# Kernel tuning notes

Measured on AMD Instinct MI355X. Metric: run time of the kernel, lower is better.

Reference implementation:

```python
import jax, jax.numpy as jnp
import numpy as np

B, L, D, K = 8, 256, 256, 64  # batch, slots, n_input, attn_dimension


def setup_inputs() -> dict:
    key = jax.random.key(0)
    k1, k2, k3 = jax.random.split(key, 3)
    inputs = jax.random.normal(k1, (B, L, D), dtype=jnp.float32)
    # torch.nn.Linear weights are [out_features, in_features]; scale to avoid tanh saturation
    W1 = jax.random.normal(k2, (K, 2 * D), dtype=jnp.float32) * (1.0 / np.sqrt(2 * D))
    W2 = jax.random.normal(k3, (1, K), dtype=jnp.float32) * (1.0 / np.sqrt(K))
    return {"inputs": inputs, "W1": W1, "W2": W2}


def reference(inputs, W1, W2):
    # CONCAT branch of SlotAttention:
    #   score[b,i,j] = W2 @ tanh(W1 @ concat(inputs[b,i], inputs[b,j]))
    # Split W1 into the halves acting on the i-part and j-part of the concat
    # (identical math, avoids materializing the [B,L,L,2D] concat tensor).
    d = inputs.shape[-1]
    W1i, W1j = W1[:, :d], W1[:, d:]
    qi = jnp.einsum('bld,kd->blk', inputs, W1i)          # [B,L,K]
    kj = jnp.einsum('bld,kd->blk', inputs, W1j)          # [B,L,K]
    h = jnp.tanh(qi[:, :, None, :] + kj[:, None, :, :])  # [B,L,L,K]
    scores = jnp.einsum('bijk,k->bij', h, W2[0])         # [B,L,L]
    attn = jax.nn.softmax(scores, axis=2)                # softmax over j
    context = jnp.einsum('bij,bjd->bid', attn, inputs)   # [B,L,D]
    return jnp.concatenate([inputs, context], axis=2)    # [B,L,2D]
```

## Files before the change

kernel.cpp:

```cpp
#include <hip/hip_runtime.h>


#define Bn 8
#define Ln 256
#define Dn 256
#define Kn 64
#define ROWS (Bn*Ln)
#define IPB 4

__global__ __launch_bounds__(128) void proj_kernel(
    const float* __restrict__ X,
    const float* __restrict__ W1,
    float* __restrict__ QK)
{
    __shared__ float Xs[4 * 256];
    const int tid = threadIdx.x;
    const int r0 = blockIdx.x * 4;

    const float4* Xg4 = (const float4*)(X + r0 * Dn);
    float4* Xs4 = (float4*)Xs;
    #pragma unroll
    for (int idx = tid; idx < 256; idx += 128) Xs4[idx] = Xg4[idx];
    __syncthreads();

    const int k = tid & 63, half = tid >> 6;
    const float4* Wrow = (const float4*)(W1 + k * (2 * Dn) + half * Dn);
    float acc[4] = {0, 0, 0, 0};
    #pragma unroll 8
    for (int d4 = 0; d4 < 64; ++d4) {
        float4 w = Wrow[d4];
        #pragma unroll
        for (int r = 0; r < 4; ++r) {
            float4 x = ((const float4*)(Xs + r * Dn))[d4];
            float a = acc[r];
            a = fmaf(w.x, x.x, a);
            a = fmaf(w.y, x.y, a);
            a = fmaf(w.z, x.z, a);
            a = fmaf(w.w, x.w, a);
            acc[r] = a;
        }
    }
    #pragma unroll
    for (int r = 0; r < 4; ++r)
        QK[(r0 + r) * 128 + tid] = __expf(2.0f * acc[r]);
}

__global__ __launch_bounds__(256) void attn_kernel(
    const float* __restrict__ X,
    const float* __restrict__ QK,
    const float* __restrict__ W2,
    float* __restrict__ out)
{
    __shared__ float eq_s[IPB * Kn];
    __shared__ float w2_s[Kn];
    __shared__ float S[Ln * IPB];
    __shared__ float4 red[4 * IPB * 64];

    const int tid = threadIdx.x;
    const int b  = blockIdx.x / (Ln / IPB);
    const int i0 = (blockIdx.x % (Ln / IPB)) * IPB;

    if (tid < Kn) w2_s[tid] = W2[tid];
    {
        int ii = tid >> 6, kk = tid & 63;
        eq_s[ii * Kn + kk] = QK[(b * Ln + i0 + ii) * 128 + kk];
    }

    float ekr[Kn];
    const float4* kj4 = (const float4*)(QK + (b * Ln + tid) * 128 + 64);
    #pragma unroll
    for (int q = 0; q < 16; ++q) {
        float4 v = kj4[q];
        ekr[q * 4 + 0] = v.x; ekr[q * 4 + 1] = v.y;
        ekr[q * 4 + 2] = v.z; ekr[q * 4 + 3] = v.w;
    }
    __syncthreads();

    float Wsum;
    {
        float v = w2_s[tid & 63];
        #pragma unroll
        for (int off = 32; off > 0; off >>= 1)
            v += __shfl_xor(v, off);
        Wsum = v;
    }

    float s[IPB] = {0, 0, 0, 0};
    const float4* w4  = (const float4*)w2_s;
    const float4* q4a = (const float4*)(eq_s);
    const float4* q4b = (const float4*)(eq_s + Kn);
    const float4* q4c = (const float4*)(eq_s + 2 * Kn);
    const float4* q4d = (const float4*)(eq_s + 3 * Kn);
    #pragma unroll
    for (int k4 = 0; k4 < 16; ++k4) {
        float4 w  = w4[k4];
        float4 q0 = q4a[k4], q1 = q4b[k4], q2 = q4c[k4], q3 = q4d[k4];
        #pragma unroll
        for (int c = 0; c < 4; ++c) {
            float ek = ekr[k4 * 4 + c];
            float wk = (c == 0) ? w.x : (c == 1) ? w.y : (c == 2) ? w.z : w.w;
            float e0 = (c == 0) ? q0.x : (c == 1) ? q0.y : (c == 2) ? q0.z : q0.w;
            float e1 = (c == 0) ? q1.x : (c == 1) ? q1.y : (c == 2) ? q1.z : q1.w;
            float e2 = (c == 0) ? q2.x : (c == 1) ? q2.y : (c == 2) ? q2.z : q2.w;
            float e3 = (c == 0) ? q3.x : (c == 1) ? q3.y : (c == 2) ? q3.z : q3.w;
            s[0] = fmaf(wk, __builtin_amdgcn_rcpf(fmaf(e0, ek, 1.0f)), s[0]);
            s[1] = fmaf(wk, __builtin_amdgcn_rcpf(fmaf(e1, ek, 1.0f)), s[1]);
            s[2] = fmaf(wk, __builtin_amdgcn_rcpf(fmaf(e2, ek, 1.0f)), s[2]);
            s[3] = fmaf(wk, __builtin_amdgcn_rcpf(fmaf(e3, ek, 1.0f)), s[3]);
        }
    }
    ((float4*)S)[tid] = make_float4(fmaf(-2.0f, s[0], Wsum),
                                    fmaf(-2.0f, s[1], Wsum),
                                    fmaf(-2.0f, s[2], Wsum),
                                    fmaf(-2.0f, s[3], Wsum));
    __syncthreads();

    {
        const int wv = tid >> 6, lane = tid & 63;
        float v0 = S[(lane      ) * IPB + wv];
        float v1 = S[(lane +  64) * IPB + wv];
        float v2 = S[(lane + 128) * IPB + wv];
        float v3 = S[(lane + 192) * IPB + wv];
        float m = fmaxf(fmaxf(v0, v1), fmaxf(v2, v3));
        #pragma unroll
        for (int off = 32; off > 0; off >>= 1)
            m = fmaxf(m, __shfl_xor(m, off));
        float e0 = __expf(v0 - m), e1 = __expf(v1 - m);
        float e2 = __expf(v2 - m), e3 = __expf(v3 - m);
        float sum = e0 + e1 + e2 + e3;
        #pragma unroll
        for (int off = 32; off > 0; off >>= 1)
            sum += __shfl_xor(sum, off);
        float inv = 1.0f / sum;
        S[(lane      ) * IPB + wv] = e0 * inv;
        S[(lane +  64) * IPB + wv] = e1 * inv;
        S[(lane + 128) * IPB + wv] = e2 * inv;
        S[(lane + 192) * IPB + wv] = e3 * inv;
    }
    __syncthreads();

    {
        const int wv = tid >> 6, lane = tid & 63;
        float4 acc0 = {0,0,0,0}, acc1 = {0,0,0,0}, acc2 = {0,0,0,0}, acc3 = {0,0,0,0};
        const float4* Xb4 = (const float4*)(X + b * Ln * Dn);
        const float4* S4  = (const float4*)S;
        const int jbase = wv * 64;
        #pragma unroll 8
        for (int jj = 0; jj < 64; ++jj) {
            int j = jbase + jj;
            float4 at = S4[j];
            float4 x  = Xb4[j * 64 + lane];
            acc0.x = fmaf(at.x, x.x, acc0.x); acc0.y = fmaf(at.x, x.y, acc0.y);
            acc0.z = fmaf(at.x, x.z, acc0.z); acc0.w = fmaf(at.x, x.w, acc0.w);
            acc1.x = fmaf(at.y, x.x, acc1.x); acc1.y = fmaf(at.y, x.y, acc1.y);
            acc1.z = fmaf(at.y, x.z, acc1.z); acc1.w = fmaf(at.y, x.w, acc1.w);
            acc2.x = fmaf(at.z, x.x, acc2.x); acc2.y = fmaf(at.z, x.y, acc2.y);
            acc2.z = fmaf(at.z, x.z, acc2.z); acc2.w = fmaf(at.z, x.w, acc2.w);
            acc3.x = fmaf(at.w, x.x, acc3.x); acc3.y = fmaf(at.w, x.y, acc3.y);
            acc3.z = fmaf(at.w, x.z, acc3.z); acc3.w = fmaf(at.w, x.w, acc3.w);
        }
        red[(wv * IPB + 0) * 64 + lane] = acc0;
        red[(wv * IPB + 1) * 64 + lane] = acc1;
        red[(wv * IPB + 2) * 64 + lane] = acc2;
        red[(wv * IPB + 3) * 64 + lane] = acc3;
    }
    __syncthreads();

    {
        const int i = tid >> 6, q = tid & 63;
        float4 p0 = red[(0 * IPB + i) * 64 + q];
        float4 p1 = red[(1 * IPB + i) * 64 + q];
        float4 p2 = red[(2 * IPB + i) * 64 + q];
        float4 p3 = red[(3 * IPB + i) * 64 + q];
        float4 c;
        c.x = (p0.x + p1.x) + (p2.x + p3.x);
        c.y = (p0.y + p1.y) + (p2.y + p3.y);
        c.z = (p0.z + p1.z) + (p2.z + p3.z);
        c.w = (p0.w + p1.w) + (p2.w + p3.w);
        const int row = b * Ln + i0 + i;
        float4 xcopy = ((const float4*)(X + row * Dn))[q];
        ((float4*)(out + row * 2 * Dn))[q]      = xcopy;
        ((float4*)(out + row * 2 * Dn + Dn))[q] = c;
    }
}

extern "C" void kernel_launch(void* const* d_in, const int* in_sizes, int n_in,
                              void* d_out, int out_size, void* d_ws, size_t ws_size,
                              hipStream_t stream) {
    const float* X  = (const float*)d_in[0];
    const float* W1 = (const float*)d_in[1];
    const float* W2 = (const float*)d_in[2];
    float* out = (float*)d_out;
    float* QK  = (float*)d_ws;

    proj_kernel<<<ROWS / 4, 128, 0, stream>>>(X, W1, QK);
    attn_kernel<<<ROWS / IPB, 256, 0, stream>>>(X, QK, W2, out);
}
```

Measured before the change: 80.48 us.

## Split attention into score kernel and tiled context GEMM kernel

Splits the fused attention kernel into a score/softmax kernel that writes the normalized attention matrix to workspace and a separate context kernel that computes attn·X over 32x32 output tiles with the attention rows staged in padded shared memory. The max-subtraction in softmax is dropped and the constant Wsum offset is folded out, since it cancels in the softmax. The goal is better reuse of X across rows in the context product than the old per-4-row scheme gave. In exchange it adds a third launch and a global round trip for the 8x256x256 attention matrix, and dropping the max-subtraction risks overflow if scores grow large.

```diff
diff --git a/kernel.cpp b/kernel.cpp
--- a/kernel.cpp
+++ b/kernel.cpp
@@ -7,6 +7,7 @@
 #define Kn 64
 #define ROWS (Bn*Ln)
 #define IPB 4
+#define ASTRIDE 260
 
 __global__ __launch_bounds__(128) void proj_kernel(
     const float* __restrict__ X,
@@ -45,16 +46,14 @@
         QK[(r0 + r) * 128 + tid] = __expf(2.0f * acc[r]);
 }
 
-__global__ __launch_bounds__(256) void attn_kernel(
-    const float* __restrict__ X,
+__global__ __launch_bounds__(256) void score_kernel(
     const float* __restrict__ QK,
     const float* __restrict__ W2,
-    float* __restrict__ out)
+    float* __restrict__ attn)
 {
     __shared__ float eq_s[IPB * Kn];
     __shared__ float w2_s[Kn];
     __shared__ float S[Ln * IPB];
-    __shared__ float4 red[4 * IPB * 64];
 
     const int tid = threadIdx.x;
     const int b  = blockIdx.x / (Ln / IPB);
@@ -75,15 +74,6 @@
         ekr[q * 4 + 2] = v.z; ekr[q * 4 + 3] = v.w;
     }
     __syncthreads();
-
-    float Wsum;
-    {
-        float v = w2_s[tid & 63];
-        #pragma unroll
-        for (int off = 32; off > 0; off >>= 1)
-            v += __shfl_xor(v, off);
-        Wsum = v;
-    }
 
     float s[IPB] = {0, 0, 0, 0};
     const float4* w4  = (const float4*)w2_s;
@@ -109,79 +99,70 @@
             s[3] = fmaf(wk, __builtin_amdgcn_rcpf(fmaf(e3, ek, 1.0f)), s[3]);
         }
     }
-    ((float4*)S)[tid] = make_float4(fmaf(-2.0f, s[0], Wsum),
-                                    fmaf(-2.0f, s[1], Wsum),
-                                    fmaf(-2.0f, s[2], Wsum),
-                                    fmaf(-2.0f, s[3], Wsum));
+    ((float4*)S)[tid] = make_float4(s[0], s[1], s[2], s[3]);
     __syncthreads();
 
     {
         const int wv = tid >> 6, lane = tid & 63;
-        float v0 = S[(lane      ) * IPB + wv];
-        float v1 = S[(lane +  64) * IPB + wv];
-        float v2 = S[(lane + 128) * IPB + wv];
-        float v3 = S[(lane + 192) * IPB + wv];
-        float m = fmaxf(fmaxf(v0, v1), fmaxf(v2, v3));
-        #pragma unroll
-        for (int off = 32; off > 0; off >>= 1)
-            m = fmaxf(m, __shfl_xor(m, off));
-        float e0 = __expf(v0 - m), e1 = __expf(v1 - m);
-        float e2 = __expf(v2 - m), e3 = __expf(v3 - m);
-        float sum = e0 + e1 + e2 + e3;
+        float e0 = __expf(-2.0f * S[(lane      ) * IPB + wv]);
+        float e1 = __expf(-2.0f * S[(lane +  64) * IPB + wv]);
+        float e2 = __expf(-2.0f * S[(lane + 128) * IPB + wv]);
+        float e3 = __expf(-2.0f * S[(lane + 192) * IPB + wv]);
+        float sum = (e0 + e1) + (e2 + e3);
         #pragma unroll
         for (int off = 32; off > 0; off >>= 1)
             sum += __shfl_xor(sum, off);
         float inv = 1.0f / sum;
-        S[(lane      ) * IPB + wv] = e0 * inv;
-        S[(lane +  64) * IPB + wv] = e1 * inv;
-        S[(lane + 128) * IPB + wv] = e2 * inv;
-        S[(lane + 192) * IPB + wv] = e3 * inv;
+        float* arow = attn + (b * Ln + i0 + wv) * Ln;
+        arow[lane      ] = e0 * inv;
+        arow[lane +  64] = e1 * inv;
+        arow[lane + 128] = e2 * inv;
+        arow[lane + 192] = e3 * inv;
+    }
+}
+
+__global__ __launch_bounds__(256) void ctx_kernel(
+    const float* __restrict__ X,
+    const float* __restrict__ attn,
+    float* __restrict__ out)
+{
+    __shared__ float As[32 * ASTRIDE];
+
+    const int tid = threadIdx.x;
+    const int bid = blockIdx.x;
+    const int b  = bid >> 6;
+    const int it = (bid >> 3) & 7;
+    const int dt = bid & 7;
+    const int i0 = it * 32, d0 = dt * 32;
+
+    const float4* Ag4 = (const float4*)(attn + (b * Ln + i0) * Ln);
+    #pragma unroll
+    for (int q = 0; q < 8; ++q) {
+        int idx = q * 256 + tid;
+        int row = idx >> 6, c4 = idx & 63;
+        *((float4*)(As + row * ASTRIDE + c4 * 4)) = Ag4[idx];
     }
     __syncthreads();
 
-    {
-        const int wv = tid >> 6, lane = tid & 63;
-        float4 acc0 = {0,0,0,0}, acc1 = {0,0,0,0}, acc2 = {0,0,0,0}, acc3 = {0,0,0,0};
-        const float4* Xb4 = (const float4*)(X + b * Ln * Dn);
-        const float4* S4  = (const float4*)S;
-        const int jbase = wv * 64;
-        #pragma unroll 8
-        for (int jj = 0; jj < 64; ++jj) {
-            int j = jbase + jj;
-            float4 at = S4[j];
-            float4 x  = Xb4[j * 64 + lane];
-            acc0.x = fmaf(at.x, x.x, acc0.x); acc0.y = fmaf(at.x, x.y, acc0.y);
-            acc0.z = fmaf(at.x, x.z, acc0.z); acc0.w = fmaf(at.x, x.w, acc0.w);
-            acc1.x = fmaf(at.y, x.x, acc1.x); acc1.y = fmaf(at.y, x.y, acc1.y);
-            acc1.z = fmaf(at.y, x.z, acc1.z); acc1.w = fmaf(at.y, x.w, acc1.w);
-            acc2.x = fmaf(at.z, x.x, acc2.x); acc2.y = fmaf(at.z, x.y, acc2.y);
-            acc2.z = fmaf(at.z, x.z, acc2.z); acc2.w = fmaf(at.z, x.w, acc2.w);
-            acc3.x = fmaf(at.w, x.x, acc3.x); acc3.y = fmaf(at.w, x.y, acc3.y);
-            acc3.z = fmaf(at.w, x.z, acc3.z); acc3.w = fmaf(at.w, x.w, acc3.w);
-        }
-        red[(wv * IPB + 0) * 64 + lane] = acc0;
-        red[(wv * IPB + 1) * 64 + lane] = acc1;
-        red[(wv * IPB + 2) * 64 + lane] = acc2;
-        red[(wv * IPB + 3) * 64 + lane] = acc3;
+    const int ii = tid >> 3, dq = tid & 7;
+    const float* Arow = As + ii * ASTRIDE;
+    const float4* Xb4 = (const float4*)(X + b * Ln * Dn) + (d0 >> 2) + dq;
+
+    float4 c = {0.f, 0.f, 0.f, 0.f};
+    #pragma unroll 4
+    for (int j = 0; j < Ln; ++j) {
+        float a  = Arow[j];
+        float4 x = Xb4[j * 64];
+        c.x = fmaf(a, x.x, c.x);
+        c.y = fmaf(a, x.y, c.y);
+        c.z = fmaf(a, x.z, c.z);
+        c.w = fmaf(a, x.w, c.w);
     }
-    __syncthreads();
 
-    {
-        const int i = tid >> 6, q = tid & 63;
-        float4 p0 = red[(0 * IPB + i) * 64 + q];
-        float4 p1 = red[(1 * IPB + i) * 64 + q];
-        float4 p2 = red[(2 * IPB + i) * 64 + q];
-        float4 p3 = red[(3 * IPB + i) * 64 + q];
-        float4 c;
-        c.x = (p0.x + p1.x) + (p2.x + p3.x);
-        c.y = (p0.y + p1.y) + (p2.y + p3.y);
-        c.z = (p0.z + p1.z) + (p2.z + p3.z);
-        c.w = (p0.w + p1.w) + (p2.w + p3.w);
-        const int row = b * Ln + i0 + i;
-        float4 xcopy = ((const float4*)(X + row * Dn))[q];
-        ((float4*)(out + row * 2 * Dn))[q]      = xcopy;
-        ((float4*)(out + row * 2 * Dn + Dn))[q] = c;
-    }
+    const int row = b * Ln + i0 + ii;
+    float4 xcopy = ((const float4*)(X + row * Dn))[(d0 >> 2) + dq];
+    ((float4*)(out + row * 2 * Dn))[(d0 >> 2) + dq]      = xcopy;
+    ((float4*)(out + row * 2 * Dn + Dn))[(d0 >> 2) + dq] = c;
 }
 
 extern "C" void kernel_launch(void* const* d_in, const int* in_sizes, int n_in,
@@ -191,8 +172,11 @@
     const float* W1 = (const float*)d_in[1];
     const float* W2 = (const float*)d_in[2];
     float* out = (float*)d_out;
-    float* QK  = (float*)d_ws;
 
-    proj_kernel<<<ROWS / 4, 128, 0, stream>>>(X, W1, QK);
-    attn_kernel<<<ROWS / IPB, 256, 0, stream>>>(X, QK, W2, out);
+    float* QK   = (float*)d_ws;
+    float* attn = (float*)((char*)d_ws + (1 << 20));
+
+    proj_kernel <<<ROWS / 4,  128, 0, stream>>>(X, W1, QK);
+    score_kernel<<<ROWS / IPB, 256, 0, stream>>>(QK, W2, attn);
+    ctx_kernel  <<<512,        256, 0, stream>>>(X, attn, out);
 }
```

New measurement: 99.28 us. 23.4% more time.
